# Kernel optimization log

Measured on AMD Instinct MI355X. Metric: run time of the kernel, lower is better.

Reference implementation:

```python
import jax, jax.numpy as jnp
import numpy as np

B, T = 64, 2048
D_RNN, D_EMB, D_ATT = 1024, 512, 128
N_FILT, KSIZE = 32, 31
PAD = (KSIZE - 1) // 2


def setup_inputs() -> dict:
    key = jax.random.key(0)
    ks = jax.random.split(key, 9)
    return {
        "attention_hidden_state": jax.random.normal(ks[0], (B, D_RNN), jnp.float32),
        "memory": jax.random.normal(ks[1], (B, T, D_EMB), jnp.float32),
        "processed_memory": jax.random.normal(ks[2], (B, T, D_ATT), jnp.float32),
        "attention_weights_cat": jax.random.uniform(ks[3], (B, 2, T), jnp.float32),
        "mask": jax.random.randint(ks[4], (B, T), 0, 2) > 0,
        # learned params (all bias-free, as in the torch module)
        "Wq": jax.random.normal(ks[5], (D_ATT, D_RNN), jnp.float32) * 0.02,   # query_layer.weight
        "Wv": jax.random.normal(ks[6], (1, D_ATT), jnp.float32) * 0.02,        # v.weight
        "conv_w": jax.random.normal(ks[7], (N_FILT, 2, KSIZE), jnp.float32) * 0.1,  # location_conv.weight (OIH)
        "Wd": jax.random.normal(ks[8], (D_ATT, N_FILT), jnp.float32) * 0.02,   # location_dense.weight
    }


def reference(attention_hidden_state, memory, processed_memory,
              attention_weights_cat, mask, Wq, Wv, conv_w, Wd):
    # processed query: [B, 1, D_ATT]
    pq = (attention_hidden_state @ Wq.T)[:, None, :]
    # location features: Conv1d(2 -> N_FILT, same padding) over time
    loc = jax.lax.conv_general_dilated(
        attention_weights_cat, conv_w,
        window_strides=(1,), padding=[(PAD, PAD)],
        dimension_numbers=("NCH", "OIH", "NCH"))           # [B, N_FILT, T]
    paw = jnp.einsum("bft,af->bta", loc, Wd)               # [B, T, D_ATT]
    # additive energies -> scalar per position via v-projection
    energies = jnp.einsum("bta,a->bt", jnp.tanh(pq + paw + processed_memory), Wv[0])
    alignment = jnp.where(mask, -jnp.inf, energies)         # masked fill
    attention_weights = jax.nn.softmax(alignment, axis=1)   # [B, T]
    attention_context = jnp.einsum("bt,btd->bd", attention_weights, memory)  # [B, D_EMB]
    return attention_context, jax.lax.stop_gradient(attention_weights)
```

## Files before the change

### kernel.cpp

```cpp
#include <hip/hip_runtime.h>
#include <math.h>

#define B_    64
#define T_    2048
#define DRNN  1024
#define DEMB  512
#define DATT  128
#define NF    32
#define KS    31
#define PADL  15
#define TT    32
#define CT    64
#define NC    (T_/CT)

__device__ __forceinline__ float fast_tanh(float x){
    float e2 = __expf(2.0f * x);
    return 1.0f - 2.0f / (e2 + 1.0f);
}

__global__ __launch_bounds__(256) void prep_kernel(
    const float* __restrict__ hidden, const float* __restrict__ Wq,
    const float* __restrict__ Wd, const float* __restrict__ convw,
    float* __restrict__ pq, float* __restrict__ M2)
{
    const int blk = blockIdx.x;
    const int tid = threadIdx.x;
    if (blk < B_) {
        const int b    = blk;
        const int lane = tid & 63;
        const int w    = tid >> 6;
        float4 h[4];
        #pragma unroll
        for (int j = 0; j < 4; ++j)
            h[j] = *(const float4*)(hidden + b*DRNN + lane*4 + j*256);
        for (int ai = 0; ai < 32; ++ai){
            const int a = w*32 + ai;
            const float4* wq4 = (const float4*)(Wq + (size_t)a*DRNN);
            float acc = 0.f;
            #pragma unroll
            for (int j = 0; j < 4; ++j){
                const float4 q = wq4[lane + j*64];
                acc = fmaf(q.x, h[j].x, acc);
                acc = fmaf(q.y, h[j].y, acc);
                acc = fmaf(q.z, h[j].z, acc);
                acc = fmaf(q.w, h[j].w, acc);
            }
            acc += __shfl_xor(acc, 1, 64);  acc += __shfl_xor(acc, 2, 64);
            acc += __shfl_xor(acc, 4, 64);  acc += __shfl_xor(acc, 8, 64);
            acc += __shfl_xor(acc, 16, 64); acc += __shfl_xor(acc, 32, 64);
            if (lane == 0) pq[b*DATT + a] = acc;
        }
    } else {
        const int a = tid & 127;
        const int h = tid >> 7;
        float wd[NF];
        #pragma unroll
        for (int f = 0; f < NF; ++f) wd[f] = Wd[a*NF + f];
        for (int ck = h*KS; ck < h*KS + KS; ++ck){
            float acc = 0.f;
            #pragma unroll
            for (int f = 0; f < NF; ++f) acc = fmaf(wd[f], convw[f*2*KS + ck], acc);
            M2[ck*DATT + a] = acc;
        }
    }
}

__global__ __launch_bounds__(256) void fused_kernel(
    const float* __restrict__ pm, const float* __restrict__ awcat,
    const float* __restrict__ pq, const float* __restrict__ M2,
    const float* __restrict__ Wv, const int* __restrict__ mask,
    const float* __restrict__ memory,
    float* __restrict__ pbuf, float* __restrict__ pmax,
    float* __restrict__ psum, float* __restrict__ pctx)
{
    const int b   = blockIdx.y;
    const int cx  = blockIdx.x;
    const int t0  = cx * CT;
    const int tid = threadIdx.x;
    const int s   = tid >> 7;
    const int a   = tid & 127;
    const int ts  = t0 + TT * s;

    __shared__ float saw0[96], saw1[96];
    __shared__ float sred[2][2][TT];
    __shared__ float2 swt[CT];
    __shared__ int   scount;
    __shared__ float4 sacc[128];
    __shared__ unsigned int smkbits[2];

    for (int i = tid; i < 94; i += 256){
        int tt = t0 - PADL + i;
        bool ok = (tt >= 0) && (tt < T_);
        saw0[i] = ok ? awcat[(b*2+0)*T_ + tt] : 0.f;
        saw1[i] = ok ? awcat[(b*2+1)*T_ + tt] : 0.f;
    }
    if (tid < 64){
        const int mk = mask[b*T_ + t0 + tid] != 0;
        const unsigned long long bal = __ballot(mk);
        if (tid == 0){
            smkbits[0] = (unsigned)bal;
            smkbits[1] = (unsigned)(bal >> 32);
        }
    }
    __syncthreads();

    const float pqa = pq[b*DATT + a];
    const float wv  = Wv[a];
    const unsigned mkb = __builtin_amdgcn_readfirstlane(smkbits[s]);

    const float* pmb = pm + ((size_t)(b*T_ + ts)) * DATT + a;
    float acc[TT];
    #pragma unroll
    for (int t = 0; t < TT; ++t){
        acc[t] = 0.f;
        if (((mkb >> t) & 1u) == 0u) acc[t] = pmb[(size_t)t * DATT];
    }

    float Ma0[KS], Ma1[KS];
    const float* M2a = M2 + a;
    #pragma unroll
    for (int k = 0; k < KS; ++k){
        Ma0[k] = M2a[(size_t)k * DATT];
        Ma1[k] = M2a[(size_t)(KS + k) * DATT];
    }

    #pragma unroll
    for (int t = 0; t < TT; ++t) acc[t] += pqa;

    #pragma unroll
    for (int j = 0; j < TT + KS - 1; ++j){
        const float av0 = saw0[j + TT*s];
        const float av1 = saw1[j + TT*s];
        const int tlo = (j - KS + 1) > 0 ? (j - KS + 1) : 0;
        const int thi = (j < TT - 1) ? j : (TT - 1);
        #pragma unroll
        for (int t = tlo; t <= thi; ++t){
            acc[t] = fmaf(Ma0[j - t], av0, acc[t]);
            acc[t] = fmaf(Ma1[j - t], av1, acc[t]);
        }
    }

    #pragma unroll
    for (int t = 0; t < TT; ++t){
        acc[t] = wv * fast_tanh(acc[t]);
    }

    const int lane = tid & 63;
    const int half = a >> 6;
    #pragma unroll
    for (int k = 0; k < 16; ++k){
        const bool hi = (lane & 1) != 0;
        float send = hi ? acc[k] : acc[k+16];
        float recv = __shfl_xor(send, 1, 64);
        acc[k] = (hi ? acc[k+16] : acc[k]) + recv;
    }
    #pragma unroll
    for (int k = 0; k < 8; ++k){
        const bool hi = (lane & 2) != 0;
        float send = hi ? acc[k] : acc[k+8];
        float recv = __shfl_xor(send, 2, 64);
        acc[k] = (hi ? acc[k+8] : acc[k]) + recv;
    }
    #pragma unroll
    for (int k = 0; k < 4; ++k){
        const bool hi = (lane & 4) != 0;
        float send = hi ? acc[k] : acc[k+4];
        float recv = __shfl_xor(send, 4, 64);
        acc[k] = (hi ? acc[k+4] : acc[k]) + recv;
    }
    #pragma unroll
    for (int k = 0; k < 2; ++k){
        const bool hi = (lane & 8) != 0;
        float send = hi ? acc[k] : acc[k+2];
        float recv = __shfl_xor(send, 8, 64);
        acc[k] = (hi ? acc[k+2] : acc[k]) + recv;
    }
    {
        const bool hi = (lane & 16) != 0;
        float send = hi ? acc[0] : acc[1];
        float recv = __shfl_xor(send, 16, 64);
        acc[0] = (hi ? acc[1] : acc[0]) + recv;
    }
    acc[0] += __shfl_xor(acc[0], 32, 64);
    const int trev = ((lane & 1) << 4) | (((lane >> 1) & 1) << 3) |
                     (((lane >> 2) & 1) << 2) | (((lane >> 3) & 1) << 1) |
                     ((lane >> 4) & 1);
    if (lane < 32) sred[s][half][trev] = acc[0];
    __syncthreads();

    if (tid < 64){
        const int t = t0 + tid;
        float e = sred[tid>>5][0][tid&31] + sred[tid>>5][1][tid&31];
        const int mk = (smkbits[tid>>5] >> (tid&31)) & 1u;
        float mval = mk ? -1e30f : e;
        #pragma unroll
        for (int off = 1; off < 64; off <<= 1) mval = fmaxf(mval, __shfl_xor(mval, off, 64));
        const float pval = mk ? 0.f : __expf(e - mval);
        float sv = pval;
        #pragma unroll
        for (int off = 1; off < 64; off <<= 1) sv += __shfl_xor(sv, off, 64);
        pbuf[b*T_ + t] = pval;
        const unsigned long long bal = __ballot(pval != 0.f);
        if (pval != 0.f){
            const int pfx = (int)__popcll(bal & ((1ull << tid) - 1ull));
            swt[pfx] = make_float2(pval, __int_as_float(tid));
        }
        if (tid == 0){
            scount = (int)__popcll(bal);
            pmax[b*NC + cx] = mval;
            psum[b*NC + cx] = sv;
        }
    }
    __syncthreads();

    const int n   = scount;
    const int col = tid & 127;
    const int row = tid >> 7;
    float4 a4 = make_float4(0.f, 0.f, 0.f, 0.f);
    const float4* mem4 = (const float4*)memory + ((size_t)(b*T_ + t0))*(DEMB/4) + col;

    int i = row;
    for (; i + 14 < n; i += 16){
        float2 e[8];
        #pragma unroll
        for (int u = 0; u < 8; ++u) e[u] = swt[i + 2*u];
        float4 m[8];
        #pragma unroll
        for (int u = 0; u < 8; ++u)
            m[u] = mem4[(size_t)__float_as_int(e[u].y) * (DEMB/4)];
        #pragma unroll
        for (int u = 0; u < 8; ++u){
            a4.x = fmaf(e[u].x, m[u].x, a4.x);
            a4.y = fmaf(e[u].x, m[u].y, a4.y);
            a4.z = fmaf(e[u].x, m[u].z, a4.z);
            a4.w = fmaf(e[u].x, m[u].w, a4.w);
        }
    }
    for (; i + 6 < n; i += 8){
        const float2 e0 = swt[i];
        const float2 e1 = swt[i+2];
        const float2 e2 = swt[i+4];
        const float2 e3 = swt[i+6];
        const float4 m0 = mem4[(size_t)__float_as_int(e0.y) * (DEMB/4)];
        const float4 m1 = mem4[(size_t)__float_as_int(e1.y) * (DEMB/4)];
        const float4 m2 = mem4[(size_t)__float_as_int(e2.y) * (DEMB/4)];
        const float4 m3 = mem4[(size_t)__float_as_int(e3.y) * (DEMB/4)];
        a4.x = fmaf(e0.x, m0.x, a4.x); a4.y = fmaf(e0.x, m0.y, a4.y);
        a4.z = fmaf(e0.x, m0.z, a4.z); a4.w = fmaf(e0.x, m0.w, a4.w);
        a4.x = fmaf(e1.x, m1.x, a4.x); a4.y = fmaf(e1.x, m1.y, a4.y);
        a4.z = fmaf(e1.x, m1.z, a4.z); a4.w = fmaf(e1.x, m1.w, a4.w);
        a4.x = fmaf(e2.x, m2.x, a4.x); a4.y = fmaf(e2.x, m2.y, a4.y);
        a4.z = fmaf(e2.x, m2.z, a4.z); a4.w = fmaf(e2.x, m2.w, a4.w);
        a4.x = fmaf(e3.x, m3.x, a4.x); a4.y = fmaf(e3.x, m3.y, a4.y);
        a4.z = fmaf(e3.x, m3.z, a4.z); a4.w = fmaf(e3.x, m3.w, a4.w);
    }
    for (; i < n; i += 2){
        const float2 e = swt[i];
        const float4 m = mem4[(size_t)__float_as_int(e.y) * (DEMB/4)];
        a4.x = fmaf(e.x, m.x, a4.x); a4.y = fmaf(e.x, m.y, a4.y);
        a4.z = fmaf(e.x, m.z, a4.z); a4.w = fmaf(e.x, m.w, a4.w);
    }

    if (row == 1) sacc[col] = a4;
    __syncthreads();
    if (row == 0){
        const float4 o = sacc[col];
        float4* dst = (float4*)(pctx + ((size_t)(b*NC + cx))*DEMB) + col;
        *dst = make_float4(a4.x + o.x, a4.y + o.y, a4.z + o.z, a4.w + o.w);
    }
}

__global__ __launch_bounds__(256) void finalize_kernel(
    const float* __restrict__ pbuf, const float* __restrict__ pmax,
    const float* __restrict__ psum, const float* __restrict__ pctx,
    float* __restrict__ ctx, float* __restrict__ wout)
{
    const int b = blockIdx.x;
    const int tid = threadIdx.x;
    __shared__ float sscale[NC];

    if (tid < 64){
        float mv = (tid < NC) ? pmax[b*NC + tid] : -1e30f;
        float sv = (tid < NC) ? psum[b*NC + tid] : 0.f;
        float g = mv;
        #pragma unroll
        for (int off = 1; off < 64; off <<= 1) g = fmaxf(g, __shfl_xor(g, off, 64));
        float z = sv * __expf(mv - g);
        #pragma unroll
        for (int off = 1; off < 64; off <<= 1) z += __shfl_xor(z, off, 64);
        if (tid < NC) sscale[tid] = __expf(mv - g) / z;
    }
    __syncthreads();

    float2 a2 = make_float2(0.f, 0.f);
    const float2* pc2 = (const float2*)(pctx + (size_t)b*NC*DEMB) + tid;
    #pragma unroll
    for (int c = 0; c < NC; ++c){
        const float sc = sscale[c];
        if (sc != 0.f){
            const float2 v = pc2[(size_t)c * (DEMB/2)];
            a2.x = fmaf(sc, v.x, a2.x);
            a2.y = fmaf(sc, v.y, a2.y);
        }
    }
    ((float2*)(ctx + b*DEMB))[tid] = a2;

    #pragma unroll
    for (int i = 0; i < T_/256; ++i){
        const int t = tid + 256*i;
        wout[b*T_ + t] = pbuf[b*T_ + t] * sscale[t >> 6];
    }
}

extern "C" void kernel_launch(void* const* d_in, const int* in_sizes, int n_in,
                              void* d_out, int out_size, void* d_ws, size_t ws_size,
                              hipStream_t stream)
{
    const float* hidden = (const float*)d_in[0];
    const float* memory = (const float*)d_in[1];
    const float* pm     = (const float*)d_in[2];
    const float* awcat  = (const float*)d_in[3];
    const int*   mask   = (const int*)d_in[4];
    const float* Wq     = (const float*)d_in[5];
    const float* Wv     = (const float*)d_in[6];
    const float* convw  = (const float*)d_in[7];
    const float* Wd     = (const float*)d_in[8];

    float* out  = (float*)d_out;
    float* ctx  = out;
    float* wout = out + B_*DEMB;

    float* pq    = (float*)d_ws;
    float* M2    = pq   + B_*DATT;
    float* pbuf  = M2   + 8192;
    float* pmax  = pbuf + B_*T_;
    float* psum  = pmax + B_*NC;
    float* pctx  = psum + B_*NC;

    prep_kernel<<<dim3(B_ + 1), 256, 0, stream>>>(hidden, Wq, Wd, convw, pq, M2);
    fused_kernel<<<dim3(NC, B_), 256, 0, stream>>>(pm, awcat, pq, M2, Wv, mask,
                                                   memory, pbuf, pmax, psum, pctx);
    finalize_kernel<<<dim3(B_), 256, 0, stream>>>(pbuf, pmax, psum, pctx, ctx, wout);
}
```

Baseline: 439.2 us.

## Retune occupancy, hoist global loads above barrier, widen prep and finalize grids

Several independent tweaks. Prep runs with 512 threads so each wave computes fewer query rows and M2 rows. The fused kernel gets a min-blocks hint of 4, computes its mask bits per wave with a ballot, and issues the processed-memory and M2 loads before the shared-memory barrier so they overlap the awcat staging. The 8-way unrolled gather loop is dropped to save registers, and finalize is split across 8 blocks per batch so more CUs share the weight rescale. Risks are register spills under the occupancy hint, plus redundant softmax-scale recomputation in every finalize block.

```diff
diff --git a/kernel.cpp b/kernel.cpp
--- a/kernel.cpp
+++ b/kernel.cpp
@@ -18,7 +18,7 @@
     return 1.0f - 2.0f / (e2 + 1.0f);
 }
 
-__global__ __launch_bounds__(256) void prep_kernel(
+__global__ __launch_bounds__(512) void prep_kernel(
     const float* __restrict__ hidden, const float* __restrict__ Wq,
     const float* __restrict__ Wd, const float* __restrict__ convw,
     float* __restrict__ pq, float* __restrict__ M2)
@@ -33,8 +33,8 @@
         #pragma unroll
         for (int j = 0; j < 4; ++j)
             h[j] = *(const float4*)(hidden + b*DRNN + lane*4 + j*256);
-        for (int ai = 0; ai < 32; ++ai){
-            const int a = w*32 + ai;
+        for (int ai = 0; ai < 16; ++ai){
+            const int a = w*16 + ai;
             const float4* wq4 = (const float4*)(Wq + (size_t)a*DRNN);
             float acc = 0.f;
             #pragma unroll
@@ -52,11 +52,13 @@
         }
     } else {
         const int a = tid & 127;
-        const int h = tid >> 7;
+        const int g = tid >> 7;
         float wd[NF];
         #pragma unroll
         for (int f = 0; f < NF; ++f) wd[f] = Wd[a*NF + f];
-        for (int ck = h*KS; ck < h*KS + KS; ++ck){
+        const int cklo = g*16;
+        const int ckhi = (g*16 + 16 < 2*KS) ? (g*16 + 16) : 2*KS;
+        for (int ck = cklo; ck < ckhi; ++ck){
             float acc = 0.f;
             #pragma unroll
             for (int f = 0; f < NF; ++f) acc = fmaf(wd[f], convw[f*2*KS + ck], acc);
@@ -65,7 +67,7 @@
     }
 }
 
-__global__ __launch_bounds__(256) void fused_kernel(
+__global__ __launch_bounds__(256, 4) void fused_kernel(
     const float* __restrict__ pm, const float* __restrict__ awcat,
     const float* __restrict__ pq, const float* __restrict__ M2,
     const float* __restrict__ Wv, const int* __restrict__ mask,
@@ -80,6 +82,7 @@
     const int s   = tid >> 7;
     const int a   = tid & 127;
     const int ts  = t0 + TT * s;
+    const int lane = tid & 63;
 
     __shared__ float saw0[96], saw1[96];
     __shared__ float sred[2][2][TT];
@@ -88,6 +91,28 @@
     __shared__ float4 sacc[128];
     __shared__ unsigned int smkbits[2];
 
+    int mymk = 0;
+    if (lane < 32) mymk = (mask[b*T_ + ts + lane] != 0);
+    const unsigned long long bal0 = __ballot(mymk);
+    const unsigned mkb = (unsigned)bal0;
+
+    const float pqa = pq[b*DATT + a];
+    const float wv  = Wv[a];
+    const float* pmb = pm + ((size_t)(b*T_ + ts)) * DATT + a;
+    float acc[TT];
+    #pragma unroll
+    for (int t = 0; t < TT; ++t){
+        acc[t] = 0.f;
+        if (((mkb >> t) & 1u) == 0u) acc[t] = pmb[(size_t)t * DATT];
+    }
+    float Ma0[KS], Ma1[KS];
+    const float* M2a = M2 + a;
+    #pragma unroll
+    for (int k = 0; k < KS; ++k){
+        Ma0[k] = M2a[(size_t)k * DATT];
+        Ma1[k] = M2a[(size_t)(KS + k) * DATT];
+    }
+
     for (int i = tid; i < 94; i += 256){
         int tt = t0 - PADL + i;
         bool ok = (tt >= 0) && (tt < T_);
@@ -104,26 +129,6 @@
     }
     __syncthreads();
 
-    const float pqa = pq[b*DATT + a];
-    const float wv  = Wv[a];
-    const unsigned mkb = __builtin_amdgcn_readfirstlane(smkbits[s]);
-
-    const float* pmb = pm + ((size_t)(b*T_ + ts)) * DATT + a;
-    float acc[TT];
-    #pragma unroll
-    for (int t = 0; t < TT; ++t){
-        acc[t] = 0.f;
-        if (((mkb >> t) & 1u) == 0u) acc[t] = pmb[(size_t)t * DATT];
-    }
-
-    float Ma0[KS], Ma1[KS];
-    const float* M2a = M2 + a;
-    #pragma unroll
-    for (int k = 0; k < KS; ++k){
-        Ma0[k] = M2a[(size_t)k * DATT];
-        Ma1[k] = M2a[(size_t)(KS + k) * DATT];
-    }
-
     #pragma unroll
     for (int t = 0; t < TT; ++t) acc[t] += pqa;
 
@@ -145,7 +150,6 @@
         acc[t] = wv * fast_tanh(acc[t]);
     }
 
-    const int lane = tid & 63;
     const int half = a >> 6;
     #pragma unroll
     for (int k = 0; k < 16; ++k){
@@ -220,22 +224,6 @@
     const float4* mem4 = (const float4*)memory + ((size_t)(b*T_ + t0))*(DEMB/4) + col;
 
     int i = row;
-    for (; i + 14 < n; i += 16){
-        float2 e[8];
-        #pragma unroll
-        for (int u = 0; u < 8; ++u) e[u] = swt[i + 2*u];
-        float4 m[8];
-        #pragma unroll
-        for (int u = 0; u < 8; ++u)
-            m[u] = mem4[(size_t)__float_as_int(e[u].y) * (DEMB/4)];
-        #pragma unroll
-        for (int u = 0; u < 8; ++u){
-            a4.x = fmaf(e[u].x, m[u].x, a4.x);
-            a4.y = fmaf(e[u].x, m[u].y, a4.y);
-            a4.z = fmaf(e[u].x, m[u].z, a4.z);
-            a4.w = fmaf(e[u].x, m[u].w, a4.w);
-        }
-    }
     for (; i + 6 < n; i += 8){
         const float2 e0 = swt[i];
         const float2 e1 = swt[i+2];
@@ -275,41 +263,39 @@
     const float* __restrict__ psum, const float* __restrict__ pctx,
     float* __restrict__ ctx, float* __restrict__ wout)
 {
-    const int b = blockIdx.x;
+    const int b   = blockIdx.y;
+    const int g   = blockIdx.x;
     const int tid = threadIdx.x;
     __shared__ float sscale[NC];
 
     if (tid < 64){
         float mv = (tid < NC) ? pmax[b*NC + tid] : -1e30f;
         float sv = (tid < NC) ? psum[b*NC + tid] : 0.f;
-        float g = mv;
-        #pragma unroll
-        for (int off = 1; off < 64; off <<= 1) g = fmaxf(g, __shfl_xor(g, off, 64));
-        float z = sv * __expf(mv - g);
+        float gm = mv;
+        #pragma unroll
+        for (int off = 1; off < 64; off <<= 1) gm = fmaxf(gm, __shfl_xor(gm, off, 64));
+        float z = sv * __expf(mv - gm);
         #pragma unroll
         for (int off = 1; off < 64; off <<= 1) z += __shfl_xor(z, off, 64);
-        if (tid < NC) sscale[tid] = __expf(mv - g) / z;
-    }
-    __syncthreads();
-
-    float2 a2 = make_float2(0.f, 0.f);
-    const float2* pc2 = (const float2*)(pctx + (size_t)b*NC*DEMB) + tid;
-    #pragma unroll
-    for (int c = 0; c < NC; ++c){
-        const float sc = sscale[c];
-        if (sc != 0.f){
+        if (tid < NC) sscale[tid] = __expf(mv - gm) / z;
+    }
+    __syncthreads();
+
+    if (g == 0){
+        float2 a2 = make_float2(0.f, 0.f);
+        const float2* pc2 = (const float2*)(pctx + (size_t)b*NC*DEMB) + tid;
+        #pragma unroll
+        for (int c = 0; c < NC; ++c){
+            const float sc = sscale[c];
             const float2 v = pc2[(size_t)c * (DEMB/2)];
             a2.x = fmaf(sc, v.x, a2.x);
             a2.y = fmaf(sc, v.y, a2.y);
         }
-    }
-    ((float2*)(ctx + b*DEMB))[tid] = a2;
-
-    #pragma unroll
-    for (int i = 0; i < T_/256; ++i){
-        const int t = tid + 256*i;
-        wout[b*T_ + t] = pbuf[b*T_ + t] * sscale[t >> 6];
-    }
+        ((float2*)(ctx + b*DEMB))[tid] = a2;
+    }
+
+    const int t = g*256 + tid;
+    wout[b*T_ + t] = pbuf[b*T_ + t] * sscale[t >> 6];
 }
 
 extern "C" void kernel_launch(void* const* d_in, const int* in_sizes, int n_in,
@@ -337,8 +323,8 @@
     float* psum  = pmax + B_*NC;
     float* pctx  = psum + B_*NC;
 
-    prep_kernel<<<dim3(B_ + 1), 256, 0, stream>>>(hidden, Wq, Wd, convw, pq, M2);
+    prep_kernel<<<dim3(B_ + 1), 512, 0, stream>>>(hidden, Wq, Wd, convw, pq, M2);
     fused_kernel<<<dim3(NC, B_), 256, 0, stream>>>(pm, awcat, pq, M2, Wv, mask,
                                                    memory, pbuf, pmax, psum, pctx);
-    finalize_kernel<<<dim3(B_), 256, 0, stream>>>(pbuf, pmax, psum, pctx, ctx, wout);
-}
+    finalize_kernel<<<dim3(8, B_), 256, 0, stream>>>(pbuf, pmax, psum, pctx, ctx, wout);
+}
```

After: 405.0 us. 7.8% less time.
